# Kernel tuning notes

Hardware: AMD Instinct MI355X
Metric: run time of the kernel (lower is better)

## Reference

```python
import jax, jax.numpy as jnp
import numpy as np

EPS_CLAMP_LO = 1e-6
EPS_CLAMP_HI = 1.0 - 1e-6
B = 262144


def _soft_perm(W):
    # minmax weight normalization per row, then row-normalize -> soft permutation
    lo = W.min(axis=1, keepdims=True)
    hi = W.max(axis=1, keepdims=True)
    Wn = (W - lo) / (hi - lo + 1e-8)
    return Wn / (Wn.sum(axis=1, keepdims=True) + 1e-8)


def setup_inputs() -> dict:
    key = jax.random.key(0)
    k1, k2, k3, k4 = jax.random.split(key, 4)
    p1 = jax.random.uniform(k1, (B, 10), dtype=jnp.float32)
    p2 = jax.random.uniform(k2, (B, 10), dtype=jnp.float32)
    W1 = jax.random.normal(k3, (10, 10), dtype=jnp.float32)
    W2 = jax.random.normal(k4, (10, 10), dtype=jnp.float32)
    return {"p1": p1, "p2": p2, "W1": W1, "W2": W2}


def reference(p1, p2, W1, W2):
    # binaryTreeLogicNet.input_to_leaf: learned soft permutation of the 10 digits
    l1 = p1 @ _soft_perm(W1).T  # [B,10]
    l2 = p2 @ _soft_perm(W2).T  # [B,10]
    # MinMaxAggregator graded AND with a=1.0 -> elementwise min over all pairs
    s = jnp.minimum(l1[:, :, None], l2[:, None, :])  # [B,10,10]
    log1m = jnp.log(1.0 - jnp.clip(s, EPS_CLAMP_LO, EPS_CLAMP_HI) + 1e-12)
    # i+j=k grouping: scatter-add expressed as one [B,100] x [100,19] matmul
    sum_idx = (jnp.arange(10)[:, None] + jnp.arange(10)[None, :]).reshape(100)
    M = jax.nn.one_hot(sum_idx, 19, dtype=log1m.dtype)  # [100,19]
    log_prod = log1m.reshape(-1, 100) @ M  # [B,19]
    y = 1.0 - jnp.exp(log_prod)  # smooth OR per sum k
    return y / (y.sum(axis=1, keepdims=True) + 1e-9)
```

## Files before the change

### kernel.cpp

```cpp
#include <hip/hip_runtime.h>

#define TPB 256

__global__ void softperm_kernel(const float* __restrict__ W1,
                                const float* __restrict__ W2,
                                float* __restrict__ P) {
    int t = threadIdx.x;
    if (t >= 20) return;
    const float* W = (t < 10) ? W1 : W2;
    int r = (t < 10) ? t : (t - 10);
    float w[10];
    float lo = 1e30f, hi = -1e30f;
#pragma unroll
    for (int j = 0; j < 10; ++j) {
        w[j] = W[r * 10 + j];
        lo = fminf(lo, w[j]);
        hi = fmaxf(hi, w[j]);
    }
    float inv = 1.0f / (hi - lo + 1e-8f);
    float s = 0.0f;
#pragma unroll
    for (int j = 0; j < 10; ++j) { w[j] = (w[j] - lo) * inv; s += w[j]; }
    float invs = 1.0f / (s + 1e-8f);
#pragma unroll
    for (int j = 0; j < 10; ++j) P[t * 10 + j] = w[j] * invs;
}

__global__ __launch_bounds__(TPB) void bacon_main(
    const float* __restrict__ p1, const float* __restrict__ p2,
    const float* __restrict__ P, float* __restrict__ out, int nrows) {
    __shared__ __align__(16) float sIn[2 * TPB * 10];

    const int tid = threadIdx.x;
    const int rowBase = blockIdx.x * TPB;
    int rowsHere = nrows - rowBase;
    if (rowsHere > TPB) rowsHere = TPB;

    {
        const int nflt = rowsHere * 10;
        const int nvec = nflt >> 2;
        const float4* g1 = (const float4*)(p1 + (size_t)rowBase * 10);
        const float4* g2 = (const float4*)(p2 + (size_t)rowBase * 10);
        float4* s1 = (float4*)sIn;
        float4* s2 = (float4*)(sIn + TPB * 10);
        for (int e = tid; e < nvec; e += TPB) {
            s1[e] = g1[e];
            s2[e] = g2[e];
        }
        for (int e = (nvec << 2) + tid; e < nflt; e += TPB) {
            sIn[e] = p1[(size_t)rowBase * 10 + e];
            sIn[TPB * 10 + e] = p2[(size_t)rowBase * 10 + e];
        }
    }
    __syncthreads();

    float y[19];
    const bool row_ok = (tid < rowsHere);
    if (row_ok) {
        float a[10], b[10];
#pragma unroll
        for (int j = 0; j < 10; ++j) {
            a[j] = sIn[tid * 10 + j];
            b[j] = sIn[TPB * 10 + tid * 10 + j];
        }
        float q[10], r[10];
#pragma unroll
        for (int i = 0; i < 10; ++i) {
            float l1 = 0.0f, l2 = 0.0f;
#pragma unroll
            for (int j = 0; j < 10; ++j) {
                l1 = fmaf(P[i * 10 + j], a[j], l1);
                l2 = fmaf(P[100 + i * 10 + j], b[j], l2);
            }
            l1 = fminf(fmaxf(l1, 1e-6f), 1.0f - 1e-6f);
            l2 = fminf(fmaxf(l2, 1e-6f), 1.0f - 1e-6f);
            q[i] = (1.0f - l1) + 1e-12f;
            r[i] = (1.0f - l2) + 1e-12f;
        }
        float pr[19];
#pragma unroll
        for (int k = 0; k < 19; ++k) pr[k] = 1.0f;
#pragma unroll
        for (int i = 0; i < 10; ++i) {
#pragma unroll
            for (int j = 0; j < 10; ++j) {
                pr[i + j] *= fmaxf(q[i], r[j]);
            }
        }
        float ssum = 0.0f;
#pragma unroll
        for (int k = 0; k < 19; ++k) {
            y[k] = 1.0f - pr[k];
            ssum += y[k];
        }
        float invs = 1.0f / (ssum + 1e-9f);
#pragma unroll
        for (int k = 0; k < 19; ++k) y[k] *= invs;
    }
    __syncthreads();

    if (row_ok) {
#pragma unroll
        for (int k = 0; k < 19; ++k) sIn[tid * 19 + k] = y[k];
    }
    __syncthreads();

    {
        const int nflt = rowsHere * 19;
        const int nvec = nflt >> 2;
        float* og = out + (size_t)rowBase * 19;
        float4* og4 = (float4*)og;
        const float4* s4 = (const float4*)sIn;
        for (int e = tid; e < nvec; e += TPB) og4[e] = s4[e];
        for (int e = (nvec << 2) + tid; e < nflt; e += TPB) og[e] = sIn[e];
    }
}

extern "C" void kernel_launch(void* const* d_in, const int* in_sizes, int n_in,
                              void* d_out, int out_size, void* d_ws, size_t ws_size,
                              hipStream_t stream) {
    const float* p1 = (const float*)d_in[0];
    const float* p2 = (const float*)d_in[1];
    const float* W1 = (const float*)d_in[2];
    const float* W2 = (const float*)d_in[3];
    float* out = (float*)d_out;
    float* P = (float*)d_ws;

    const int nrows = in_sizes[0] / 10;

    softperm_kernel<<<1, 64, 0, stream>>>(W1, W2, P);
    const int blocks = (nrows + TPB - 1) / TPB;
    bacon_main<<<blocks, TPB, 0, stream>>>(p1, p2, P, out, nrows);
}
```

Before: 81.15 us.

## Fuse soft-permutation into main kernel via algebraic row-normalization factoring

Removes the separate softperm kernel launch and workspace. Each block computes per-row min and a combined normalization factor for W1 and W2 in shared memory. The matvec then uses raw W with the correction l = (W·a - lo*sum(a)) * R, which needs the row sums of the inputs. This saves a kernel launch and the dependency between the two kernels, but every block redundantly recomputes the 20 row stats and the rearranged math may round slightly differently.

```diff
diff --git a/kernel.cpp b/kernel.cpp
--- a/kernel.cpp
+++ b/kernel.cpp
@@ -2,34 +2,12 @@
 
 #define TPB 256
 
-__global__ void softperm_kernel(const float* __restrict__ W1,
-                                const float* __restrict__ W2,
-                                float* __restrict__ P) {
-    int t = threadIdx.x;
-    if (t >= 20) return;
-    const float* W = (t < 10) ? W1 : W2;
-    int r = (t < 10) ? t : (t - 10);
-    float w[10];
-    float lo = 1e30f, hi = -1e30f;
-#pragma unroll
-    for (int j = 0; j < 10; ++j) {
-        w[j] = W[r * 10 + j];
-        lo = fminf(lo, w[j]);
-        hi = fmaxf(hi, w[j]);
-    }
-    float inv = 1.0f / (hi - lo + 1e-8f);
-    float s = 0.0f;
-#pragma unroll
-    for (int j = 0; j < 10; ++j) { w[j] = (w[j] - lo) * inv; s += w[j]; }
-    float invs = 1.0f / (s + 1e-8f);
-#pragma unroll
-    for (int j = 0; j < 10; ++j) P[t * 10 + j] = w[j] * invs;
-}
-
-__global__ __launch_bounds__(TPB) void bacon_main(
+__global__ __launch_bounds__(TPB) void bacon_fused(
     const float* __restrict__ p1, const float* __restrict__ p2,
-    const float* __restrict__ P, float* __restrict__ out, int nrows) {
+    const float* __restrict__ W1, const float* __restrict__ W2,
+    float* __restrict__ out, int nrows) {
     __shared__ __align__(16) float sIn[2 * TPB * 10];
+    __shared__ float sC[40];
 
     const int tid = threadIdx.x;
     const int rowBase = blockIdx.x * TPB;
@@ -52,26 +30,48 @@
             sIn[TPB * 10 + e] = p2[(size_t)rowBase * 10 + e];
         }
     }
+
+    if (tid < 20) {
+        const float* W = (tid < 10) ? W1 : W2;
+        const int r = (tid < 10) ? tid : (tid - 10);
+        float lo = 1e30f, hi = -1e30f, sw = 0.0f;
+#pragma unroll
+        for (int j = 0; j < 10; ++j) {
+            float w = W[r * 10 + j];
+            lo = fminf(lo, w);
+            hi = fmaxf(hi, w);
+            sw += w;
+        }
+        float R = 1.0f / ((sw - 10.0f * lo) + 1e-8f * ((hi - lo) + 1e-8f));
+        const int base = (tid < 10) ? 0 : 20;
+        sC[base + r] = lo;
+        sC[base + 10 + r] = R;
+    }
     __syncthreads();
 
     float y[19];
     const bool row_ok = (tid < rowsHere);
     if (row_ok) {
         float a[10], b[10];
+        float sa = 0.0f, sb = 0.0f;
 #pragma unroll
         for (int j = 0; j < 10; ++j) {
             a[j] = sIn[tid * 10 + j];
             b[j] = sIn[TPB * 10 + tid * 10 + j];
+            sa += a[j];
+            sb += b[j];
         }
         float q[10], r[10];
 #pragma unroll
         for (int i = 0; i < 10; ++i) {
-            float l1 = 0.0f, l2 = 0.0f;
+            float d1 = 0.0f, d2 = 0.0f;
 #pragma unroll
             for (int j = 0; j < 10; ++j) {
-                l1 = fmaf(P[i * 10 + j], a[j], l1);
-                l2 = fmaf(P[100 + i * 10 + j], b[j], l2);
+                d1 = fmaf(W1[i * 10 + j], a[j], d1);
+                d2 = fmaf(W2[i * 10 + j], b[j], d2);
             }
+            float l1 = (d1 - sC[i] * sa) * sC[10 + i];
+            float l2 = (d2 - sC[20 + i] * sb) * sC[30 + i];
             l1 = fminf(fmaxf(l1, 1e-6f), 1.0f - 1e-6f);
             l2 = fminf(fmaxf(l2, 1e-6f), 1.0f - 1e-6f);
             q[i] = (1.0f - l1) + 1e-12f;
@@ -124,11 +124,8 @@
     const float* W1 = (const float*)d_in[2];
     const float* W2 = (const float*)d_in[3];
     float* out = (float*)d_out;
-    float* P = (float*)d_ws;
 
     const int nrows = in_sizes[0] / 10;
-
-    softperm_kernel<<<1, 64, 0, stream>>>(W1, W2, P);
     const int blocks = (nrows + TPB - 1) / TPB;
-    bacon_main<<<blocks, TPB, 0, stream>>>(p1, p2, P, out, nrows);
+    bacon_fused<<<blocks, TPB, 0, stream>>>(p1, p2, W1, W2, out, nrows);
 }
```

New measurement: 79.97 us. No clear change (-1.5%).
